# Performance work log

Measured on AMD Instinct MI355X. Metric: run time of the kernel, lower is better.

## Reference

```python
import jax, jax.numpy as jnp
import numpy as np

B, L, H, T = 128, 256, 1024, 9


def setup_inputs() -> dict:
    key = jax.random.key(0)
    ks = jax.random.split(key, 7)
    hidden = jax.random.normal(ks[0], (B, L, H), dtype=jnp.float32)
    W = jax.random.normal(ks[1], (T, H), dtype=jnp.float32) * 0.02  # nn.Linear weight (T, H)
    b = jnp.zeros((T,), dtype=jnp.float32)
    start_transitions = jax.random.normal(ks[2], (T,), dtype=jnp.float32) * 0.1
    end_transitions = jax.random.normal(ks[3], (T,), dtype=jnp.float32) * 0.1
    transitions = jax.random.normal(ks[4], (T, T), dtype=jnp.float32) * 0.1
    labels = jax.random.randint(ks[5], (B, L), 0, T, dtype=jnp.int32)
    lengths = jax.random.randint(ks[6], (B,), 1, L + 1, dtype=jnp.int32)
    return dict(hidden=hidden, W=W, b=b, start_transitions=start_transitions,
                end_transitions=end_transitions, transitions=transitions,
                labels=labels, lengths=lengths)


def _crf_nll(emissions, tags, mask, start_t, end_t, trans):
    """pytorch-crf forward(): mean log-likelihood, negated.
    emissions: (B,L,T) float; tags: (B,L) int; mask: (B,L) bool with mask[:,0]=True.
    """
    Bsz = emissions.shape[0]
    maskf = mask.astype(emissions.dtype)
    bar = jnp.arange(Bsz)
    # ---- numerator: score of the gold path ----
    t0 = tags[:, 0]
    num = start_t[t0] + emissions[bar, 0, t0]
    prev, cur = tags[:, :-1], tags[:, 1:]
    em_tag = jnp.take_along_axis(emissions[:, 1:, :], cur[:, :, None], axis=2)[:, :, 0]
    num = num + jnp.sum((trans[prev, cur] + em_tag) * maskf[:, 1:], axis=1)
    seq_ends = jnp.sum(mask.astype(jnp.int32), axis=1) - 1
    last_tags = tags[bar, seq_ends]
    num = num + end_t[last_tags]
    # ---- denominator: log-partition via forward algorithm (lax.scan over time) ----
    score0 = start_t[None, :] + emissions[:, 0, :]                 # (B,T)
    em_rest = jnp.transpose(emissions[:, 1:, :], (1, 0, 2))        # (L-1,B,T)
    m_rest = jnp.transpose(mask[:, 1:], (1, 0))                    # (L-1,B)

    def step(score, xs):
        em_t, m_t = xs
        nxt = jax.nn.logsumexp(score[:, :, None] + trans[None, :, :] + em_t[:, None, :], axis=1)
        return jnp.where(m_t[:, None], nxt, score), None

    score, _ = jax.lax.scan(step, score0, (em_rest, m_rest))
    denom = jax.nn.logsumexp(score + end_t[None, :], axis=1)
    llh = num - denom
    return -jnp.mean(llh)  # reduction='mean', loss = -log_likelihood


def reference(hidden, W, b, start_transitions, end_transitions, transitions, labels, lengths):
    # dropout is identity in eval; classifier linear -> emissions
    emissions = jnp.einsum('blh,th->blt', hidden, W) + b
    mask = jnp.arange(L)[None, :] < lengths[:, None]
    mask = mask.at[:, 0].set(True)  # crf_mask[:, 0] = True
    return _crf_nll(emissions, labels, mask, start_transitions, end_transitions, transitions)
```

## Files before the change

kernel.cpp:

```cpp
#include <hip/hip_runtime.h>
#include <math.h>

#define Bn 128
#define Ln 256
#define Hn 1024
#define Tn 9
#define NROWS (Bn * Ln)
#define NTILE (NROWS / 16)
#define EMN   (NROWS * Tn)

typedef short short8 __attribute__((ext_vector_type(8)));
typedef float f32x4  __attribute__((ext_vector_type(4)));
typedef int   i32x4  __attribute__((ext_vector_type(4)));

__device__ __forceinline__ unsigned cvt_pk_bf16(float a, float b) {
  unsigned r;
  asm("v_cvt_pk_bf16_f32 %0, %1, %2" : "=v"(r) : "v"(a), "v"(b));
  return r;
}

__device__ __forceinline__ short8 pack_bf16x8(float4 lo, float4 hi) {
  i32x4 u;
  u[0] = cvt_pk_bf16(lo.x, lo.y);
  u[1] = cvt_pk_bf16(lo.z, lo.w);
  u[2] = cvt_pk_bf16(hi.x, hi.y);
  u[3] = cvt_pk_bf16(hi.z, hi.w);
  return __builtin_bit_cast(short8, u);
}

__global__ __launch_bounds__(256, 4) void emis_mfma_kernel(
    const float* __restrict__ hidden, const float* __restrict__ W,
    float* __restrict__ part)
{
  const int lane = threadIdx.x & 63;
  const int wid  = blockIdx.x * 4 + (threadIdx.x >> 6);
  const int s    = wid & 3;
  const int tile = wid >> 2;
  const int col  = lane & 15;
  const int g    = lane >> 4;

  short8 bfrag[8];
  if (col < Tn) {
    const float* wr = W + col * Hn + s * 256 + g * 8;
#pragma unroll
    for (int m = 0; m < 8; ++m) {
      float4 lo = *(const float4*)(wr + m * 32);
      float4 hi = *(const float4*)(wr + m * 32 + 4);
      bfrag[m] = pack_bf16x8(lo, hi);
    }
  } else {
#pragma unroll
    for (int m = 0; m < 8; ++m) bfrag[m] = (short8)0;
  }

  const float* A = hidden + (size_t)tile * 16 * Hn + (size_t)col * Hn + s * 256 + g * 8;
  float4 lo[8], hi[8];
#pragma unroll
  for (int m = 0; m < 8; ++m) {
    lo[m] = *(const float4*)(A + m * 32);
    hi[m] = *(const float4*)(A + m * 32 + 4);
  }
  f32x4 acc = {0.f, 0.f, 0.f, 0.f};
#pragma unroll
  for (int m = 0; m < 8; ++m) {
    short8 af = pack_bf16x8(lo[m], hi[m]);
    acc = __builtin_amdgcn_mfma_f32_16x16x32_bf16(af, bfrag[m], acc, 0, 0, 0);
  }

  if (col < Tn) {
    float* p = part + (size_t)s * EMN;
    const int rbase = tile * 16 + g * 4;
#pragma unroll
    for (int r = 0; r < 4; ++r)
      p[(size_t)(rbase + r) * Tn + col] = acc[r];
  }
}

__global__ __launch_bounds__(256) void combine_kernel(
    const float* __restrict__ part, const float* __restrict__ bias,
    float* __restrict__ em)
{
  const int i = blockIdx.x * 256 + threadIdx.x;
  float v = part[i] + part[i + EMN] + part[i + 2 * EMN] + part[i + 3 * EMN];
  em[i] = v + bias[i % Tn];
}

__global__ __launch_bounds__(64) void crfA_kernel(
    const float* __restrict__ em, const int* __restrict__ lengths,
    const float* __restrict__ trans, float* __restrict__ M)
{
  const int bid = blockIdx.x;
  const int b = bid / 72, rem = bid % 72, c = rem / 9, s0 = rem % 9;
  const int lane = threadIdx.x;
  const int j = (lane < Tn) ? lane : 0;
  const int len = lengths[b];
  int lo = c * 32; if (lo < 1) lo = 1;
  int hi = c * 32 + 32; if (hi > len) hi = len;

  float trc[9];
#pragma unroll
  for (int i = 0; i < 9; ++i) trc[i] = trans[i * Tn + j];

  float score = (j == s0) ? 0.f : -1.0e30f;
  const float* emb = em + (size_t)b * Ln * Tn;
  for (int t = lo; t < hi; ++t) {
    const float e = emb[t * Tn + j];
    float a[9];
#pragma unroll
    for (int i = 0; i < 9; ++i) a[i] = __shfl(score, i, 64) + trc[i];
    float mx = a[0];
#pragma unroll
    for (int i = 1; i < 9; ++i) mx = fmaxf(mx, a[i]);
    float ssum = 0.f;
#pragma unroll
    for (int i = 0; i < 9; ++i) ssum += __expf(a[i] - mx);
    score = mx + __logf(ssum) + e;
  }
  if (lane < Tn)
    M[((size_t)(b * 8 + c) * 9 + s0) * 9 + lane] = score;
}

__global__ __launch_bounds__(64) void crfB_kernel(
    const float* __restrict__ em, const int* __restrict__ labels,
    const int* __restrict__ lengths, const float* __restrict__ start_t,
    const float* __restrict__ end_t, const float* __restrict__ trans,
    const float* __restrict__ M, float* __restrict__ llh)
{
  const int b = blockIdx.x, lane = threadIdx.x;
  const int len = lengths[b];
  const float* emb = em + (size_t)b * Ln * Tn;
  const int* tg = labels + b * Ln;

  float part = 0.f;
  for (int t = lane; t < len; t += 64) {
    const int cur = tg[t];
    float v = (t == 0) ? (start_t[cur] + emb[cur])
                       : (trans[tg[t - 1] * Tn + cur] + emb[t * Tn + cur]);
    if (t == len - 1) v += end_t[cur];
    part += v;
  }
#pragma unroll
  for (int m = 1; m < 64; m <<= 1) part += __shfl_xor(part, m, 64);
  const float num = part;

  const int j = (lane < Tn) ? lane : 0;
  float v = start_t[j] + emb[j];
#pragma unroll
  for (int c = 0; c < 8; ++c) {
    const float* Mc = M + (size_t)(b * 8 + c) * 81;
    float a[9];
#pragma unroll
    for (int i = 0; i < 9; ++i) a[i] = __shfl(v, i, 64) + Mc[i * 9 + j];
    float mx = a[0];
#pragma unroll
    for (int i = 1; i < 9; ++i) mx = fmaxf(mx, a[i]);
    float ssum = 0.f;
#pragma unroll
    for (int i = 0; i < 9; ++i) ssum += __expf(a[i] - mx);
    v = mx + __logf(ssum);
  }
  float fin = (lane < Tn) ? (v + end_t[j]) : -1.0e30f;
  float mx = fin;
#pragma unroll
  for (int m = 1; m < 64; m <<= 1) mx = fmaxf(mx, __shfl_xor(mx, m, 64));
  float se = __expf(fin - mx);
#pragma unroll
  for (int m = 1; m < 64; m <<= 1) se += __shfl_xor(se, m, 64);
  const float denom = mx + __logf(se);
  if (lane == 0) llh[b] = num - denom;
}

__global__ __launch_bounds__(64) void reduce_kernel(
    const float* __restrict__ llh, float* __restrict__ out)
{
  const int lane = threadIdx.x;
  float v = llh[lane] + llh[lane + 64];
#pragma unroll
  for (int m = 1; m < 64; m <<= 1) v += __shfl_xor(v, m, 64);
  if (lane == 0) out[0] = -v * (1.0f / Bn);
}

extern "C" void kernel_launch(void* const* d_in, const int* in_sizes, int n_in,
                              void* d_out, int out_size, void* d_ws, size_t ws_size,
                              hipStream_t stream) {
  const float* hidden  = (const float*)d_in[0];
  const float* W       = (const float*)d_in[1];
  const float* bias    = (const float*)d_in[2];
  const float* start_t = (const float*)d_in[3];
  const float* end_t   = (const float*)d_in[4];
  const float* trans   = (const float*)d_in[5];
  const int*   labels  = (const int*)d_in[6];
  const int*   lengths = (const int*)d_in[7];

  float* out  = (float*)d_out;
  float* wsf  = (float*)d_ws;
  float* part = wsf;
  float* em   = part + 4 * (size_t)EMN;
  float* M    = em + (size_t)EMN;
  float* llh  = M + (size_t)Bn * 8 * 81;

  emis_mfma_kernel<<<NTILE, 256, 0, stream>>>(hidden, W, part);
  combine_kernel<<<EMN / 256, 256, 0, stream>>>(part, bias, em);
  crfA_kernel<<<Bn * 8 * 9, 64, 0, stream>>>(em, lengths, trans, M);
  crfB_kernel<<<Bn, 64, 0, stream>>>(em, labels, lengths, start_t, end_t, trans, M, llh);
  reduce_kernel<<<1, 64, 0, stream>>>(llh, out);
}
```

Before: 246.3 us.

## Fuse split-K emission GEMM with combine, pack CRF chunk tasks per wave

The emission GEMM no longer splits K across four waves and writes partial sums. Each wave now covers the full K=1024 for a 16-row tile with double-buffered register loads, adds the bias and writes emissions directly, so the combine kernel and its partial-sum round trip are gone. The CRF chunk scan moves from 8 chunks of 32 steps, one task per 64-lane block, to 16 chunks of 16 steps with 7 tasks packed per wave using 9-lane groups. This shortens the serial dependency chain and raises lane utilisation, at the cost of a longer reduction in crfB and fewer resident waves doing long K loops in the GEMM.

```diff
diff --git a/kernel.cpp b/kernel.cpp
--- a/kernel.cpp
+++ b/kernel.cpp
@@ -6,8 +6,10 @@
 #define Hn 1024
 #define Tn 9
 #define NROWS (Bn * Ln)
-#define NTILE (NROWS / 16)
 #define EMN   (NROWS * Tn)
+#define NC    16
+#define CW    16
+#define NTASK (Bn * NC * 9)
 
 typedef short short8 __attribute__((ext_vector_type(8)));
 typedef float f32x4  __attribute__((ext_vector_type(4)));
@@ -28,96 +30,100 @@
   return __builtin_bit_cast(short8, u);
 }
 
-__global__ __launch_bounds__(256, 4) void emis_mfma_kernel(
+#define LOADC(P, cc)                                         \
+  P##A0 = *(const float4*)(Ap + (cc)*64);                    \
+  P##A1 = *(const float4*)(Ap + (cc)*64 + 4);                \
+  P##A2 = *(const float4*)(Ap + (cc)*64 + 32);               \
+  P##A3 = *(const float4*)(Ap + (cc)*64 + 36);               \
+  P##B0 = *(const float4*)(Bp + (cc)*64);                    \
+  P##B1 = *(const float4*)(Bp + (cc)*64 + 4);                \
+  P##B2 = *(const float4*)(Bp + (cc)*64 + 32);               \
+  P##B3 = *(const float4*)(Bp + (cc)*64 + 36);
+
+#define COMPC(P)                                             \
+  acc = __builtin_amdgcn_mfma_f32_16x16x32_bf16(             \
+      pack_bf16x8(P##A0, P##A1), pack_bf16x8(P##B0, P##B1), acc, 0, 0, 0); \
+  acc = __builtin_amdgcn_mfma_f32_16x16x32_bf16(             \
+      pack_bf16x8(P##A2, P##A3), pack_bf16x8(P##B2, P##B3), acc, 0, 0, 0);
+
+__global__ __launch_bounds__(256, 2) void emis_kernel(
     const float* __restrict__ hidden, const float* __restrict__ W,
-    float* __restrict__ part)
+    const float* __restrict__ bias, float* __restrict__ em)
 {
   const int lane = threadIdx.x & 63;
-  const int wid  = blockIdx.x * 4 + (threadIdx.x >> 6);
-  const int s    = wid & 3;
-  const int tile = wid >> 2;
+  const int tile = blockIdx.x * 4 + (threadIdx.x >> 6);
   const int col  = lane & 15;
   const int g    = lane >> 4;
-
-  short8 bfrag[8];
+  const int wrow = (col < Tn) ? col : (Tn - 1);
+
+  const float* Ap = hidden + ((size_t)tile * 16 + col) * Hn + g * 8;
+  const float* Bp = W + (size_t)wrow * Hn + g * 8;
+
+  float4 xA0, xA1, xA2, xA3, xB0, xB1, xB2, xB3;
+  float4 yA0, yA1, yA2, yA3, yB0, yB1, yB2, yB3;
+  f32x4 acc = {0.f, 0.f, 0.f, 0.f};
+
+  LOADC(x, 0)
+#pragma unroll
+  for (int c = 0; c < 16; c += 2) {
+    if (c + 1 < 16) { LOADC(y, c + 1) }
+    COMPC(x)
+    if (c + 2 < 16) { LOADC(x, c + 2) }
+    COMPC(y)
+  }
+
   if (col < Tn) {
-    const float* wr = W + col * Hn + s * 256 + g * 8;
-#pragma unroll
-    for (int m = 0; m < 8; ++m) {
-      float4 lo = *(const float4*)(wr + m * 32);
-      float4 hi = *(const float4*)(wr + m * 32 + 4);
-      bfrag[m] = pack_bf16x8(lo, hi);
-    }
-  } else {
-#pragma unroll
-    for (int m = 0; m < 8; ++m) bfrag[m] = (short8)0;
-  }
-
-  const float* A = hidden + (size_t)tile * 16 * Hn + (size_t)col * Hn + s * 256 + g * 8;
-  float4 lo[8], hi[8];
-#pragma unroll
-  for (int m = 0; m < 8; ++m) {
-    lo[m] = *(const float4*)(A + m * 32);
-    hi[m] = *(const float4*)(A + m * 32 + 4);
-  }
-  f32x4 acc = {0.f, 0.f, 0.f, 0.f};
-#pragma unroll
-  for (int m = 0; m < 8; ++m) {
-    short8 af = pack_bf16x8(lo[m], hi[m]);
-    acc = __builtin_amdgcn_mfma_f32_16x16x32_bf16(af, bfrag[m], acc, 0, 0, 0);
-  }
-
-  if (col < Tn) {
-    float* p = part + (size_t)s * EMN;
+    const float bcol = bias[col];
     const int rbase = tile * 16 + g * 4;
 #pragma unroll
     for (int r = 0; r < 4; ++r)
-      p[(size_t)(rbase + r) * Tn + col] = acc[r];
-  }
-}
-
-__global__ __launch_bounds__(256) void combine_kernel(
-    const float* __restrict__ part, const float* __restrict__ bias,
-    float* __restrict__ em)
-{
-  const int i = blockIdx.x * 256 + threadIdx.x;
-  float v = part[i] + part[i + EMN] + part[i + 2 * EMN] + part[i + 3 * EMN];
-  em[i] = v + bias[i % Tn];
+      em[(size_t)(rbase + r) * Tn + col] = acc[r] + bcol;
+  }
 }
 
 __global__ __launch_bounds__(64) void crfA_kernel(
     const float* __restrict__ em, const int* __restrict__ lengths,
     const float* __restrict__ trans, float* __restrict__ M)
 {
-  const int bid = blockIdx.x;
-  const int b = bid / 72, rem = bid % 72, c = rem / 9, s0 = rem % 9;
   const int lane = threadIdx.x;
-  const int j = (lane < Tn) ? lane : 0;
-  const int len = lengths[b];
-  int lo = c * 32; if (lo < 1) lo = 1;
-  int hi = c * 32 + 32; if (hi > len) hi = len;
+  const int g = lane / 9;
+  const int j = lane - g * 9;
+  const int task0 = blockIdx.x * 7 + g;
+  const bool act = (g < 7) && (task0 < NTASK);
+  const int task = act ? task0 : 0;
+  const int c  = task / (Bn * 9);
+  const int rr = task - c * (Bn * 9);
+  const int b  = rr / 9;
+  const int s0 = rr - b * 9;
+  int len = act ? lengths[b] : 0;
+
+  int lo = c * CW; if (lo < 1) lo = 1;
+  int hi = c * CW + CW; if (hi > len) hi = len;
 
   float trc[9];
 #pragma unroll
   for (int i = 0; i < 9; ++i) trc[i] = trans[i * Tn + j];
 
+  const float* emb = em + (size_t)b * Ln * Tn;
   float score = (j == s0) ? 0.f : -1.0e30f;
-  const float* emb = em + (size_t)b * Ln * Tn;
+  const int base = g * 9;
+
   for (int t = lo; t < hi; ++t) {
     const float e = emb[t * Tn + j];
     float a[9];
 #pragma unroll
-    for (int i = 0; i < 9; ++i) a[i] = __shfl(score, i, 64) + trc[i];
+    for (int i = 0; i < 9; ++i) a[i] = __shfl(score, base + i, 64) + trc[i];
     float mx = a[0];
 #pragma unroll
     for (int i = 1; i < 9; ++i) mx = fmaxf(mx, a[i]);
-    float ssum = 0.f;
-#pragma unroll
-    for (int i = 0; i < 9; ++i) ssum += __expf(a[i] - mx);
-    score = mx + __logf(ssum) + e;
-  }
-  if (lane < Tn)
-    M[((size_t)(b * 8 + c) * 9 + s0) * 9 + lane] = score;
+    float s = 0.f;
+#pragma unroll
+    for (int i = 0; i < 9; ++i) s += __expf(a[i] - mx);
+    score = mx + __logf(s) + e;
+  }
+
+  if (act)
+    M[(size_t)(b * NC + c) * 81 + s0 * 9 + j] = score;
 }
 
 __global__ __launch_bounds__(64) void crfB_kernel(
@@ -146,18 +152,18 @@
   const int j = (lane < Tn) ? lane : 0;
   float v = start_t[j] + emb[j];
 #pragma unroll
-  for (int c = 0; c < 8; ++c) {
-    const float* Mc = M + (size_t)(b * 8 + c) * 81;
+  for (int c = 0; c < NC; ++c) {
+    const float* Mc = M + (size_t)(b * NC + c) * 81;
     float a[9];
 #pragma unroll
     for (int i = 0; i < 9; ++i) a[i] = __shfl(v, i, 64) + Mc[i * 9 + j];
     float mx = a[0];
 #pragma unroll
     for (int i = 1; i < 9; ++i) mx = fmaxf(mx, a[i]);
-    float ssum = 0.f;
-#pragma unroll
-    for (int i = 0; i < 9; ++i) ssum += __expf(a[i] - mx);
-    v = mx + __logf(ssum);
+    float s = 0.f;
+#pragma unroll
+    for (int i = 0; i < 9; ++i) s += __expf(a[i] - mx);
+    v = mx + __logf(s);
   }
   float fin = (lane < Tn) ? (v + end_t[j]) : -1.0e30f;
   float mx = fin;
@@ -192,16 +198,14 @@
   const int*   labels  = (const int*)d_in[6];
   const int*   lengths = (const int*)d_in[7];
 
-  float* out  = (float*)d_out;
-  float* wsf  = (float*)d_ws;
-  float* part = wsf;
-  float* em   = part + 4 * (size_t)EMN;
-  float* M    = em + (size_t)EMN;
-  float* llh  = M + (size_t)Bn * 8 * 81;
-
-  emis_mfma_kernel<<<NTILE, 256, 0, stream>>>(hidden, W, part);
-  combine_kernel<<<EMN / 256, 256, 0, stream>>>(part, bias, em);
-  crfA_kernel<<<Bn * 8 * 9, 64, 0, stream>>>(em, lengths, trans, M);
+  float* out = (float*)d_out;
+  float* wsf = (float*)d_ws;
+  float* em  = wsf;
+  float* M   = em + (size_t)EMN;
+  float* llh = M + (size_t)Bn * NC * 81;
+
+  emis_kernel<<<NROWS / 16 / 4, 256, 0, stream>>>(hidden, W, bias, em);
+  crfA_kernel<<<(NTASK + 6) / 7, 64, 0, stream>>>(em, lengths, trans, M);
   crfB_kernel<<<Bn, 64, 0, stream>>>(em, labels, lengths, start_t, end_t, trans, M, llh);
   reduce_kernel<<<1, 64, 0, stream>>>(llh, out);
 }
```

New measurement: 231.9 us. 1.06x faster.
